# Optimization experiments

Measured on AMD Instinct MI355X. Metric: run time of the kernel, lower is better.

## Reference

```python
import jax, jax.numpy as jnp
import numpy as np

NO_LANE = 90  # sentinel label meaning 'no lane'

def smooth_l1(x):
    ax = jnp.abs(x)
    return jnp.where(ax < 1.0, 0.5 * x * x, ax - 0.5)

def setup_inputs() -> dict:
    key = jax.random.key(0)
    ks = jax.random.split(key, 10)
    B, M, T, L, NL, P = 32768, 6, 30, 10, 10, 50
    cls_ = jax.random.normal(ks[0], (B, M), dtype=jnp.float32)
    reg = jax.random.normal(ks[1], (B, M, T, 2), dtype=jnp.float32) * 5.0
    lane_cls = jax.random.normal(ks[2], (B, L), dtype=jnp.float32)
    gt_preds = jax.random.normal(ks[3], (B, T, 2), dtype=jnp.float32) * 5.0
    rot = jax.random.normal(ks[4], (B, 2, 2), dtype=jnp.float32)
    orig = jax.random.normal(ks[5], (B, 2), dtype=jnp.float32)
    lane_feats = jax.random.normal(ks[6], (B, NL, P, 2), dtype=jnp.float32) * 5.0
    has_preds = jax.random.uniform(ks[7], (B, T)) < 0.8
    has_preds = has_preds.at[:, 0].set(True)  # ensure mask = max_last > 1.0 holds for every row
    lane_labels = jax.random.randint(ks[8], (B,), 0, L, dtype=jnp.int32)
    lane_labels = jnp.where(jax.random.uniform(ks[9], (B,)) < 0.05, NO_LANE, lane_labels)
    return dict(cls=cls_, reg=reg, lane_cls=lane_cls, gt_preds=gt_preds, rot=rot,
                orig=orig, lane_feats=lane_feats, has_preds=has_preds, lane_labels=lane_labels)

def reference(cls, reg, lane_cls, gt_preds, rot, orig, lane_feats, has_preds, lane_labels):
    B, M, T, _ = reg.shape
    rows = jnp.arange(B)
    hasf = has_preds.astype(jnp.float32)

    # last valid timestep per agent (argmax of has + tiny time ramp)
    last = hasf + 0.1 * jnp.arange(T, dtype=jnp.float32) / T
    last_idcs = jnp.argmax(last, axis=1)
    mask = jnp.max(last, axis=1) > 1.0  # [B], all True by construction
    maskf = mask.astype(jnp.float32)

    # endpoint distance per mode -> min mode selection
    end_reg = reg[rows, :, last_idcs]            # [B, M, 2]
    end_gt = gt_preds[rows, last_idcs]           # [B, 2]
    dist = jnp.sqrt(((end_reg - end_gt[:, None, :]) ** 2).sum(-1))  # [B, M]
    min_idcs = jnp.argmin(dist, axis=1)

    # classification target: mode with min total squared error
    cls_tar = jnp.argmin(((reg - gt_preds[:, None]) ** 2).sum(-1).sum(-1), axis=1)
    nll = -jnp.take_along_axis(jax.nn.log_softmax(cls, axis=-1), cls_tar[:, None], axis=1)[:, 0]
    cls_loss = (nll * maskf).sum() / jnp.maximum(maskf.sum(), 1.0)  # CE mean over masked rows

    reg_sel = reg[rows, min_idcs]                # [B, T, 2]
    w_reg = hasf * maskf[:, None]
    reg_loss = (smooth_l1(reg_sel - gt_preds) * w_reg[:, :, None]).sum()
    num_reg = w_reg.sum()

    # lane classification: per-sample CE * (label+1), skipping sentinel
    valid = lane_labels != NO_LANE
    validf = valid.astype(jnp.float32)
    lab_c = jnp.where(valid, lane_labels, 0)
    lane_nll = -jnp.take_along_axis(jax.nn.log_softmax(lane_cls, axis=-1), lab_c[:, None], axis=1)[:, 0]
    lane_cls_loss = (lane_nll * (lab_c.astype(jnp.float32) + 1.0) * validf).sum()
    num_lane_cls = validf.sum()

    # lane-offset loss: lane polyline in global frame, point-to-lane min distances
    lane_sel = lane_feats[rows, lab_c]           # [B, P, 2]
    lane_w = jnp.einsum('bpc,bcd->bpd', lane_sel, rot) + orig[:, None, :]
    d_reg = jnp.linalg.norm(lane_w[:, None, :, :] - reg_sel[:, :, None, :], axis=-1).min(-1)  # [B, T]
    d_gt = jnp.linalg.norm(lane_w[:, None, :, :] - gt_preds[:, :, None, :], axis=-1).min(-1)  # [B, T]
    diff = d_reg - d_gt
    check = (d_reg >= d_gt).astype(jnp.float32)
    per = (diff * check * hasf).sum(1) / jnp.maximum(hasf.sum(1), 1.0)  # mean over valid steps
    w_off = validf * maskf
    lane_off_loss = (per * w_off).sum()
    num_lane_off = w_off.sum()

    return jnp.stack([cls_loss, maskf.sum() * 0 + 1.0, reg_loss, num_reg,
                      lane_cls_loss, num_lane_cls, lane_off_loss, num_lane_off])
```

## Files before the change

kernel.cpp:

```cpp
#include <hip/hip_runtime.h>
#include <math.h>

#define NO_LANE 90
constexpr int Bt  = 32768;
constexpr int Mm  = 6;
constexpr int Tt  = 30;
constexpr int Ll  = 10;
constexpr int NLl = 10;
constexpr int Pp  = 50;

constexpr int BPB  = 8;
constexpr int NBLK = Bt / BPB;

constexpr int RPAD = 368;
constexpr int GPAD = 64;
constexpr int LPAD = 104;

__device__ __forceinline__ float smoothl1(float x) {
    float ax = fabsf(x);
    return ax < 1.0f ? 0.5f * x * x : ax - 0.5f;
}

__global__ void detect_fmt(const unsigned int* __restrict__ hp_words,
                           unsigned int* __restrict__ cnt) {
    unsigned int s = 0;
    for (int i = threadIdx.x; i < 1024; i += 256) {
        unsigned int u = hp_words[i];
        s += (u & 0xFFu) + ((u >> 8) & 0xFFu) + ((u >> 16) & 0xFFu) + (u >> 24);
    }
    for (int o = 32; o; o >>= 1) s += __shfl_down(s, o);
    if ((threadIdx.x & 63) == 0) atomicAdd(cnt, s);
}

__global__ __launch_bounds__(256) void pred_loss_main(
    const float* __restrict__ cls, const float* __restrict__ reg,
    const float* __restrict__ lane_cls, const float* __restrict__ gt,
    const float* __restrict__ rot, const float* __restrict__ orig,
    const float* __restrict__ lane_feats, const unsigned char* __restrict__ hp,
    const int* __restrict__ lane_labels, const unsigned int* __restrict__ cnt,
    float* __restrict__ partials, float* __restrict__ accum, int use_partials) {

    __shared__ __align__(16) float sReg[BPB][RPAD];
    __shared__ __align__(16) float sGt[BPB][GPAD];
    __shared__ __align__(16) float sLW[BPB][LPAD];
    __shared__ float sPart[BPB][8];

    const int tid = threadIdx.x;
    const int sb  = tid >> 5;
    const int l   = tid & 31;
    const int h   = (tid >> 5) & 1;
    const int b   = blockIdx.x * BPB + sb;

    const unsigned int c = *cnt;
    const bool byte_fmt = (c > 2000u && c < 10000u);

    bool has = false;
    if (l < Tt) {
        int idx = b * Tt + l;
        has = byte_fmt ? (hp[idx] != 0)
                       : (((const unsigned int*)hp)[idx] != 0u);
    }
    unsigned long long ball = __ballot(has);
    unsigned int mmask = (unsigned int)(ball >> (h * 32));
    int   last  = 31 - __clz((int)(mmask | 1u));
    float maskf = (mmask >> 1) ? 1.0f : 0.0f;
    float n_has = (float)__popc((int)mmask);
    float hasf  = has ? 1.0f : 0.0f;

    int   lab    = lane_labels[b];
    bool  valid  = (lab != NO_LANE);
    int   lab_c  = valid ? lab : 0;
    float validf = valid ? 1.0f : 0.0f;

    const float4* regv = (const float4*)(reg + (size_t)b * (Mm * Tt * 2));
    float4* sRegV = (float4*)&sReg[sb][0];
    sRegV[l]      = regv[l];
    sRegV[l + 32] = regv[l + 32];
    if (l < 26) sRegV[l + 64] = regv[l + 64];
    if (l < 15)
        ((float4*)&sGt[sb][0])[l] = ((const float4*)(gt + (size_t)b * (Tt * 2)))[l];

    float4 R = *(const float4*)(rot + (size_t)b * 4);
    float2 O = *(const float2*)(orig + (size_t)b * 2);
    if (l < 25) {
        float4 ls = ((const float4*)(lane_feats +
                     ((size_t)b * NLl + lab_c) * (Pp * 2)))[l];
        float4 lw;
        lw.x = ls.x * R.x + ls.y * R.z + O.x;
        lw.y = ls.x * R.y + ls.y * R.w + O.y;
        lw.z = ls.z * R.x + ls.w * R.z + O.x;
        lw.w = ls.z * R.y + ls.w * R.w + O.y;
        ((float4*)&sLW[sb][0])[l] = lw;
    }

    float cm = (l < Mm) ? cls[(size_t)b * Mm + l] : -INFINITY;
    float lc = (l < Ll) ? lane_cls[(size_t)b * Ll + l] : -INFINITY;

    __syncthreads();

    float pm[Mm];
#pragma unroll
    for (int m = 0; m < Mm; ++m) pm[m] = 0.f;
    float gx = 0.f, gy = 0.f;
    if (l < Tt) {
        gx = sGt[sb][2 * l];
        gy = sGt[sb][2 * l + 1];
#pragma unroll
        for (int m = 0; m < Mm; ++m) {
            float dx = sReg[sb][m * 60 + 2 * l] - gx;
            float dy = sReg[sb][m * 60 + 2 * l + 1] - gy;
            pm[m] = dx * dx + dy * dy;
        }
    }
#pragma unroll
    for (int m = 0; m < Mm; ++m)
#pragma unroll
        for (int o = 16; o; o >>= 1) pm[m] += __shfl_xor(pm[m], o);
    int cls_tar = 0;
    float bestc = pm[0];
#pragma unroll
    for (int m = 1; m < Mm; ++m)
        if (pm[m] < bestc) { bestc = pm[m]; cls_tar = m; }

    float egx = sGt[sb][2 * last], egy = sGt[sb][2 * last + 1];
    int   min_i = 0;
    float bd = INFINITY;
#pragma unroll
    for (int m = 0; m < Mm; ++m) {
        float dx = sReg[sb][m * 60 + 2 * last] - egx;
        float dy = sReg[sb][m * 60 + 2 * last + 1] - egy;
        float d2 = dx * dx + dy * dy;
        if (d2 < bd) { bd = d2; min_i = m; }
    }

    float mx = cm;
#pragma unroll
    for (int o = 4; o; o >>= 1) mx = fmaxf(mx, __shfl_xor(mx, o));
    float ex = (l < Mm) ? __expf(cm - mx) : 0.f;
#pragma unroll
    for (int o = 4; o; o >>= 1) ex += __shfl_xor(ex, o);
    float ctar = __shfl(cm, cls_tar + h * 32);
    float nll  = mx + __logf(ex) - ctar;

    float mx2 = lc;
#pragma unroll
    for (int o = 8; o; o >>= 1) mx2 = fmaxf(mx2, __shfl_xor(mx2, o));
    float ex2 = (l < Ll) ? __expf(lc - mx2) : 0.f;
#pragma unroll
    for (int o = 8; o; o >>= 1) ex2 += __shfl_xor(ex2, o);
    float ltar = __shfl(lc, lab_c + h * 32);
    float lnll = mx2 + __logf(ex2) - ltar;

    float regl = 0.f;
    float rsx = 0.f, rsy = 0.f;
    if (l < Tt) {
        rsx = sReg[sb][min_i * 60 + 2 * l];
        rsy = sReg[sb][min_i * 60 + 2 * l + 1];
        regl = (smoothl1(rsx - gx) + smoothl1(rsy - gy)) * hasf * maskf;
    }
#pragma unroll
    for (int o = 16; o; o >>= 1) regl += __shfl_xor(regl, o);

    float dminR = INFINITY, dminG = INFINITY;
    const float4* lw4 = (const float4*)&sLW[sb][0];
#pragma unroll
    for (int j = 0; j < 25; ++j) {
        float4 q = lw4[j];
        float ax0 = q.x - rsx, ay0 = q.y - rsy;
        float ax1 = q.z - rsx, ay1 = q.w - rsy;
        dminR = fminf(dminR, fminf(ax0 * ax0 + ay0 * ay0, ax1 * ax1 + ay1 * ay1));
        float bx0 = q.x - gx, by0 = q.y - gy;
        float bx1 = q.z - gx, by1 = q.w - gy;
        dminG = fminf(dminG, fminf(bx0 * bx0 + by0 * by0, bx1 * bx1 + by1 * by1));
    }
    float pern = 0.f;
    if (l < Tt) {
        float dr = sqrtf(dminR), dg = sqrtf(dminG);
        pern = (dr >= dg) ? (dr - dg) * hasf : 0.f;
    }
#pragma unroll
    for (int o = 16; o; o >>= 1) pern += __shfl_xor(pern, o);

    if (l == 0) {
        float per = pern / fmaxf(n_has, 1.0f);
        sPart[sb][0] = nll * maskf;
        sPart[sb][1] = maskf;
        sPart[sb][2] = regl;
        sPart[sb][3] = maskf * n_has;
        sPart[sb][4] = lnll * (float)(lab_c + 1) * validf;
        sPart[sb][5] = validf;
        sPart[sb][6] = per * validf * maskf;
        sPart[sb][7] = validf * maskf;
    }
    __syncthreads();
    if (tid < 8) {
        float s = 0.f;
#pragma unroll
        for (int k = 0; k < BPB; ++k) s += sPart[k][tid];
        if (use_partials)
            partials[(size_t)blockIdx.x * 8 + tid] = s;
        else
            atomicAdd(accum + tid, s);
    }
}

__global__ __launch_bounds__(1024) void finalize_k(const float* __restrict__ partials,
                                                   float* __restrict__ out, int nb) {
    int c  = threadIdx.x & 7;
    int i0 = threadIdx.x >> 3;
    float s = 0.f;
    for (int k = i0; k < nb; k += 128) s += partials[(size_t)k * 8 + c];
    __shared__ float red[1024];
    red[threadIdx.x] = s;
    __syncthreads();
    for (int off = 512; off >= 8; off >>= 1) {
        if ((int)threadIdx.x < off) red[threadIdx.x] += red[threadIdx.x + off];
        __syncthreads();
    }
    if (threadIdx.x == 0) {
        out[0] = red[0] / fmaxf(red[1], 1.0f);
        out[1] = 1.0f;
        out[2] = red[2];
        out[3] = red[3];
        out[4] = red[4];
        out[5] = red[5];
        out[6] = red[6];
        out[7] = red[7];
    }
}

extern "C" void kernel_launch(void* const* d_in, const int* in_sizes, int n_in,
                              void* d_out, int out_size, void* d_ws, size_t ws_size,
                              hipStream_t stream) {
    const float* cls        = (const float*)d_in[0];
    const float* reg        = (const float*)d_in[1];
    const float* lane_cls   = (const float*)d_in[2];
    const float* gt         = (const float*)d_in[3];
    const float* rot        = (const float*)d_in[4];
    const float* orig       = (const float*)d_in[5];
    const float* lane_feats = (const float*)d_in[6];
    const unsigned char* hp = (const unsigned char*)d_in[7];
    const int* lane_labels  = (const int*)d_in[8];
    float* out = (float*)d_out;

    unsigned int* cnt = (unsigned int*)d_ws;
    float* accum      = (float*)((char*)d_ws + 16);
    float* partials   = (float*)((char*)d_ws + 256);
    size_t need = 256 + (size_t)NBLK * 8 * sizeof(float);
    int use_partials = (ws_size >= need) ? 1 : 0;

    hipMemsetAsync(d_ws, 0, 64, stream);
    detect_fmt<<<1, 256, 0, stream>>>((const unsigned int*)hp, cnt);
    pred_loss_main<<<NBLK, 256, 0, stream>>>(
        cls, reg, lane_cls, gt, rot, orig, lane_feats, hp, lane_labels, cnt,
        partials, accum, use_partials);
    finalize_k<<<1, 1024, 0, stream>>>(use_partials ? partials : accum, out,
                                       use_partials ? NBLK : 1);
}
```

Measured before the change: 238.1 us.

## Fuse format detection and final reduction into single main kernel launch

Removes the separate format-detection kernel and the finalize kernel. Each block now recomputes the byte-format check from the first 256 bytes of has_preds via a wave shuffle. Per-block sums go into 64 atomic slots, and the last block (found with a done counter) reduces the slots and writes the output. This cuts two kernel launches and their serialization. In exchange it adds a global atomic counter, fences, and atomic contention on the slots.

```diff
diff --git a/kernel.cpp b/kernel.cpp
--- a/kernel.cpp
+++ b/kernel.cpp
@@ -9,8 +9,9 @@
 constexpr int NLl = 10;
 constexpr int Pp  = 50;
 
-constexpr int BPB  = 8;
-constexpr int NBLK = Bt / BPB;
+constexpr int BPB   = 8;
+constexpr int NBLK  = Bt / BPB;
+constexpr int NSLOT = 64;
 
 constexpr int RPAD = 368;
 constexpr int GPAD = 64;
@@ -21,29 +22,21 @@
     return ax < 1.0f ? 0.5f * x * x : ax - 0.5f;
 }
 
-__global__ void detect_fmt(const unsigned int* __restrict__ hp_words,
-                           unsigned int* __restrict__ cnt) {
-    unsigned int s = 0;
-    for (int i = threadIdx.x; i < 1024; i += 256) {
-        unsigned int u = hp_words[i];
-        s += (u & 0xFFu) + ((u >> 8) & 0xFFu) + ((u >> 16) & 0xFFu) + (u >> 24);
-    }
-    for (int o = 32; o; o >>= 1) s += __shfl_down(s, o);
-    if ((threadIdx.x & 63) == 0) atomicAdd(cnt, s);
-}
-
-__global__ __launch_bounds__(256) void pred_loss_main(
+__global__ __launch_bounds__(256) void pred_loss_fused(
     const float* __restrict__ cls, const float* __restrict__ reg,
     const float* __restrict__ lane_cls, const float* __restrict__ gt,
     const float* __restrict__ rot, const float* __restrict__ orig,
     const float* __restrict__ lane_feats, const unsigned char* __restrict__ hp,
-    const int* __restrict__ lane_labels, const unsigned int* __restrict__ cnt,
-    float* __restrict__ partials, float* __restrict__ accum, int use_partials) {
+    const int* __restrict__ lane_labels,
+    unsigned int* __restrict__ done, float* __restrict__ slots,
+    float* __restrict__ out) {
 
     __shared__ __align__(16) float sReg[BPB][RPAD];
     __shared__ __align__(16) float sGt[BPB][GPAD];
     __shared__ __align__(16) float sLW[BPB][LPAD];
     __shared__ float sPart[BPB][8];
+    __shared__ float sRed[8];
+    __shared__ int   sLast;
 
     const int tid = threadIdx.x;
     const int sb  = tid >> 5;
@@ -51,8 +44,12 @@
     const int h   = (tid >> 5) & 1;
     const int b   = blockIdx.x * BPB + sb;
 
-    const unsigned int c = *cnt;
-    const bool byte_fmt = (c > 2000u && c < 10000u);
+    unsigned int u = ((const unsigned int*)hp)[tid & 63];
+    unsigned int s = (u & 0xFFu) + ((u >> 8) & 0xFFu) +
+                     ((u >> 16) & 0xFFu) + (u >> 24);
+#pragma unroll
+    for (int o = 32; o; o >>= 1) s += __shfl_xor((int)s, o);
+    const bool byte_fmt = (s > 100u && s < 2000u);
 
     bool has = false;
     if (l < Tt) {
@@ -193,39 +190,35 @@
         sPart[sb][7] = validf * maskf;
     }
     __syncthreads();
+
     if (tid < 8) {
-        float s = 0.f;
-#pragma unroll
-        for (int k = 0; k < BPB; ++k) s += sPart[k][tid];
-        if (use_partials)
-            partials[(size_t)blockIdx.x * 8 + tid] = s;
-        else
-            atomicAdd(accum + tid, s);
-    }
-}
-
-__global__ __launch_bounds__(1024) void finalize_k(const float* __restrict__ partials,
-                                                   float* __restrict__ out, int nb) {
-    int c  = threadIdx.x & 7;
-    int i0 = threadIdx.x >> 3;
-    float s = 0.f;
-    for (int k = i0; k < nb; k += 128) s += partials[(size_t)k * 8 + c];
-    __shared__ float red[1024];
-    red[threadIdx.x] = s;
-    __syncthreads();
-    for (int off = 512; off >= 8; off >>= 1) {
-        if ((int)threadIdx.x < off) red[threadIdx.x] += red[threadIdx.x + off];
+        float sum = 0.f;
+#pragma unroll
+        for (int k = 0; k < BPB; ++k) sum += sPart[k][tid];
+        atomicAdd(&slots[(size_t)(blockIdx.x & (NSLOT - 1)) * 16 + tid], sum);
+    }
+    __syncthreads();
+
+    if (tid == 0) {
+        __threadfence();
+        unsigned int prev = atomicAdd(done, 1u);
+        sLast = (prev == (unsigned int)(NBLK - 1)) ? 1 : 0;
+    }
+    __syncthreads();
+    if (sLast) {
+        __threadfence();
+        if (tid < 8) {
+            float tot = 0.f;
+            for (int k = 0; k < NSLOT; ++k)
+                tot += __hip_atomic_load(&slots[(size_t)k * 16 + tid],
+                                         __ATOMIC_RELAXED,
+                                         __HIP_MEMORY_SCOPE_AGENT);
+            sRed[tid] = tot;
+        }
         __syncthreads();
-    }
-    if (threadIdx.x == 0) {
-        out[0] = red[0] / fmaxf(red[1], 1.0f);
-        out[1] = 1.0f;
-        out[2] = red[2];
-        out[3] = red[3];
-        out[4] = red[4];
-        out[5] = red[5];
-        out[6] = red[6];
-        out[7] = red[7];
+        if (tid == 0) out[0] = sRed[0] / fmaxf(sRed[1], 1.0f);
+        else if (tid == 1) out[1] = 1.0f;
+        else if (tid < 8) out[tid] = sRed[tid];
     }
 }
 
@@ -243,17 +236,11 @@
     const int* lane_labels  = (const int*)d_in[8];
     float* out = (float*)d_out;
 
-    unsigned int* cnt = (unsigned int*)d_ws;
-    float* accum      = (float*)((char*)d_ws + 16);
-    float* partials   = (float*)((char*)d_ws + 256);
-    size_t need = 256 + (size_t)NBLK * 8 * sizeof(float);
-    int use_partials = (ws_size >= need) ? 1 : 0;
-
-    hipMemsetAsync(d_ws, 0, 64, stream);
-    detect_fmt<<<1, 256, 0, stream>>>((const unsigned int*)hp, cnt);
-    pred_loss_main<<<NBLK, 256, 0, stream>>>(
-        cls, reg, lane_cls, gt, rot, orig, lane_feats, hp, lane_labels, cnt,
-        partials, accum, use_partials);
-    finalize_k<<<1, 1024, 0, stream>>>(use_partials ? partials : accum, out,
-                                       use_partials ? NBLK : 1);
+    unsigned int* done = (unsigned int*)d_ws;
+    float* slots = (float*)((char*)d_ws + 64);
+
+    hipMemsetAsync(d_ws, 0, 64 + NSLOT * 16 * sizeof(float), stream);
+    pred_loss_fused<<<NBLK, 256, 0, stream>>>(
+        cls, reg, lane_cls, gt, rot, orig, lane_feats, hp, lane_labels,
+        done, slots, out);
 }
```

Measured after the change: 321.2 us. 1.35x slower.
